# Optimization experiments

Measured on AMD Instinct MI355X. Metric: run time of the kernel, lower is better.

Reference implementation:

```python
import jax, jax.numpy as jnp
import numpy as np

B, T = 256, 512          # sequences, timesteps (batched over pyro.markov loop)
DATA_DIM = 88            # piano-roll tones
HIDDEN_DIM = 16          # HMM latent states
NN_DIM = 48
NN_CHANNELS = 2
KERNEL = 3


def _uniform(key, shape, fan_in):
    bound = 1.0 / np.sqrt(fan_in)
    return jax.random.uniform(key, shape, minval=-bound, maxval=bound, dtype=jnp.float32)


def setup_inputs() -> dict:
    key = jax.random.key(0)
    ks = jax.random.split(key, 13)
    w = jax.random.randint(ks[0], (B, T, 1), 0, HIDDEN_DIM)
    x = jax.random.randint(ks[1], (B, T, 1), 0, HIDDEN_DIM)
    y = jax.random.uniform(ks[2], (B, T, DATA_DIM), dtype=jnp.float32)
    return {
        "w": w, "x": x, "y": y,
        # nn.Linear(hidden_dim, nn_dim) for x and w one-hots
        "W_xh": _uniform(ks[3], (NN_DIM, HIDDEN_DIM), HIDDEN_DIM),
        "b_xh": _uniform(ks[4], (NN_DIM,), HIDDEN_DIM),
        "W_wh": _uniform(ks[5], (NN_DIM, HIDDEN_DIM), HIDDEN_DIM),
        "b_wh": _uniform(ks[6], (NN_DIM,), HIDDEN_DIM),
        # nn.Linear(nn_channels*data_dim, nn_dim)
        "W_yh": _uniform(ks[7], (NN_DIM, NN_CHANNELS * DATA_DIM), NN_CHANNELS * DATA_DIM),
        "b_yh": _uniform(ks[8], (NN_DIM,), NN_CHANNELS * DATA_DIM),
        # nn.Conv1d(1, nn_channels, 3, padding=1)
        "W_conv": _uniform(ks[9], (NN_CHANNELS, 1, KERNEL), KERNEL),
        "b_conv": _uniform(ks[10], (NN_CHANNELS,), KERNEL),
        # nn.Linear(nn_dim, data_dim)
        "W_hl": _uniform(ks[11], (DATA_DIM, NN_DIM), NN_DIM),
        "b_hl": _uniform(ks[12], (DATA_DIM,), NN_DIM),
    }


def _tones_generator(w, x, y, W_xh, b_xh, W_wh, b_wh, W_yh, b_yh, W_conv, b_conv, W_hl, b_hl):
    b, t, d = y.shape
    # one-hot scatter of the latent state indices (trailing index dim of size 1)
    w_onehot = jax.nn.one_hot(w[..., 0], HIDDEN_DIM, dtype=y.dtype)   # [B,T,H]
    x_onehot = jax.nn.one_hot(x[..., 0], HIDDEN_DIM, dtype=y.dtype)   # [B,T,H]
    # Conv1d(1 -> nn_channels, k=3, pad=1) over the tone axis
    y_nch = y.reshape(b * t, 1, d)                                    # [BT,1,D]
    y_conv = jax.lax.conv_general_dilated(
        y_nch, W_conv, window_strides=(1,), padding=[(1, 1)],
        dimension_numbers=("NCH", "OIH", "NCH"))
    y_conv = jax.nn.relu(y_conv + b_conv[None, :, None])              # [BT,C,D]
    y_conv = y_conv.reshape(b, t, NN_CHANNELS * d)                    # [B,T,C*D]
    h = jax.nn.relu(
        jnp.einsum("bth,nh->btn", x_onehot, W_xh) + b_xh
        + jnp.einsum("bth,nh->btn", w_onehot, W_wh) + b_wh
        + jnp.einsum("btc,nc->btn", y_conv, W_yh) + b_yh)             # [B,T,ND]
    return jnp.einsum("btn,dn->btd", h, W_hl) + b_hl                  # [B,T,D]


def reference(w, x, y, W_xh, b_xh, W_wh, b_wh, W_yh, b_yh, W_conv, b_conv, W_hl, b_hl):
    return _tones_generator(w, x, y, W_xh, b_xh, W_wh, b_wh, W_yh, b_yh,
                            W_conv, b_conv, W_hl, b_hl)
```

## Files before the change

### kernel.cpp

```cpp
#include <hip/hip_runtime.h>
#include <stdint.h>

#define NTOK (256 * 512)
#define TPB 256

typedef short bf16x8 __attribute__((ext_vector_type(8)));
typedef float f32x4 __attribute__((ext_vector_type(4)));
typedef unsigned short u16;
typedef unsigned int u32;

#define B1_U16 10752
#define B2_U16 6144

__device__ __forceinline__ u16 f2bf(float f) {
    u32 u = __float_as_uint(f);
    return (u16)((u + 0x7fffu + ((u >> 16) & 1u)) >> 16);
}

__global__ __launch_bounds__(256, 1)
void prep_weights(const float* __restrict__ Wxh, const float* __restrict__ bxh,
                  const float* __restrict__ Wwh, const float* __restrict__ bwh,
                  const float* __restrict__ Wyh, const float* __restrict__ byh,
                  const float* __restrict__ Whl, const float* __restrict__ bhl,
                  u16* __restrict__ ws)
{
    int e = blockIdx.x * 256 + threadIdx.x;
    if (e < B1_U16) {
        int j = e & 7, n = (e >> 3) % 48, kc = e / 384;
        int k = kc * 8 + j;
        float v;
        if (k < 176)       v = Wyh[n * 176 + (k & 1) * 88 + (k >> 1)];
        else if (k < 192)  v = Wxh[n * 16 + (k - 176)];
        else if (k < 208)  v = Wwh[n * 16 + (k - 192)];
        else if (k == 208) v = bxh[n] + bwh[n] + byh[n];
        else               v = 0.0f;
        ws[e] = f2bf(v);
    } else if (e < B1_U16 + B2_U16) {
        int e2 = e - B1_U16;
        int j = e2 & 7, dd = (e2 >> 3) % 96, kc = e2 / 768;
        int k = kc * 8 + j;
        float v = 0.0f;
        if (dd < 88) {
            if (k < 48)       v = Whl[dd * 48 + k];
            else if (k == 48) v = bhl[dd];
        }
        ws[e] = f2bf(v);
    }
}

__global__ __launch_bounds__(256, 2)
void tones_v5(const int* __restrict__ widx, const int* __restrict__ xidx,
              const float* __restrict__ y,
              const float* __restrict__ Wconv, const float* __restrict__ bconv,
              const u16* __restrict__ wsb,
              float* __restrict__ out)
{
    __shared__ __align__(16) u16 sH[4 * 1024];

    const int tid = threadIdx.x;
    const int wave = tid >> 6, lane = tid & 63;
    const int q = lane >> 4, c = lane & 15;

    bf16x8 B1[7][3];
    #pragma unroll
    for (int ks = 0; ks < 7; ks++)
        #pragma unroll
        for (int nt = 0; nt < 3; nt++)
            B1[ks][nt] = *(const bf16x8*)(wsb + ((ks * 4 + q) * 48 + nt * 16 + c) * 8);
    bf16x8 B2[2][6];
    #pragma unroll
    for (int ks = 0; ks < 2; ks++)
        #pragma unroll
        for (int nt = 0; nt < 6; nt++)
            B2[ks][nt] = *(const bf16x8*)(wsb + B1_U16 + ((ks * 4 + q) * 96 + nt * 16 + c) * 8);

    const float wc00 = Wconv[0], wc01 = Wconv[1], wc02 = Wconv[2];
    const float wc10 = Wconv[3], wc11 = Wconv[4], wc12 = Wconv[5];
    const float bc0 = bconv[0], bc1 = bconv[1];

    u16* sW = sH + wave * 1024;

    #pragma unroll 1
    for (int t = 0; t < 4; t++) {
        const int tb = blockIdx.x * 256 + wave * 64 + t * 16;
        const float* yc = y + (size_t)(tb + c) * 88;
        const int xv = xidx[tb + c];
        const int wv = widx[tb + c];

        f32x4 h0 = {0, 0, 0, 0}, h1 = {0, 0, 0, 0}, h2 = {0, 0, 0, 0};

        #pragma unroll
        for (int s = 0; s < 5; s++) {
            const int d0 = 16 * s + 4 * q;
            float p0 = (d0 == 0) ? 0.0f : yc[d0 - 1];
            float4 v4 = *(const float4*)(yc + d0);
            float p5 = yc[d0 + 4];
            float p[6] = {p0, v4.x, v4.y, v4.z, v4.w, p5};
            bf16x8 af;
            #pragma unroll
            for (int i = 0; i < 4; i++) {
                float c0 = fmaf(wc00, p[i], fmaf(wc01, p[i + 1], fmaf(wc02, p[i + 2], bc0)));
                float c1 = fmaf(wc10, p[i], fmaf(wc11, p[i + 1], fmaf(wc12, p[i + 2], bc1)));
                af[2 * i]     = (short)f2bf(fmaxf(c0, 0.0f));
                af[2 * i + 1] = (short)f2bf(fmaxf(c1, 0.0f));
            }
            h0 = __builtin_amdgcn_mfma_f32_16x16x32_bf16(af, B1[s][0], h0, 0, 0, 0);
            h1 = __builtin_amdgcn_mfma_f32_16x16x32_bf16(af, B1[s][1], h1, 0, 0, 0);
            h2 = __builtin_amdgcn_mfma_f32_16x16x32_bf16(af, B1[s][2], h2, 0, 0, 0);
        }
        {
            bf16x8 af;
            if (q < 2) {
                const int d0 = 80 + 4 * q;
                float p0 = yc[d0 - 1];
                float4 v4 = *(const float4*)(yc + d0);
                float p5 = (q == 0) ? yc[84] : 0.0f;
                float p[6] = {p0, v4.x, v4.y, v4.z, v4.w, p5};
                #pragma unroll
                for (int i = 0; i < 4; i++) {
                    float c0 = fmaf(wc00, p[i], fmaf(wc01, p[i + 1], fmaf(wc02, p[i + 2], bc0)));
                    float c1 = fmaf(wc10, p[i], fmaf(wc11, p[i + 1], fmaf(wc12, p[i + 2], bc1)));
                    af[2 * i]     = (short)f2bf(fmaxf(c0, 0.0f));
                    af[2 * i + 1] = (short)f2bf(fmaxf(c1, 0.0f));
                }
            } else {
                const int base = (q - 2) * 8;
                #pragma unroll
                for (int j = 0; j < 8; j++)
                    af[j] = (short)((base + j == xv) ? 0x3F80 : 0);
            }
            h0 = __builtin_amdgcn_mfma_f32_16x16x32_bf16(af, B1[5][0], h0, 0, 0, 0);
            h1 = __builtin_amdgcn_mfma_f32_16x16x32_bf16(af, B1[5][1], h1, 0, 0, 0);
            h2 = __builtin_amdgcn_mfma_f32_16x16x32_bf16(af, B1[5][2], h2, 0, 0, 0);
        }
        {
            bf16x8 af;
            if (q < 2) {
                const int base = q * 8;
                #pragma unroll
                for (int j = 0; j < 8; j++)
                    af[j] = (short)((base + j == wv) ? 0x3F80 : 0);
            } else {
                #pragma unroll
                for (int j = 0; j < 8; j++)
                    af[j] = (short)((q == 2 && j == 0) ? 0x3F80 : 0);
            }
            h0 = __builtin_amdgcn_mfma_f32_16x16x32_bf16(af, B1[6][0], h0, 0, 0, 0);
            h1 = __builtin_amdgcn_mfma_f32_16x16x32_bf16(af, B1[6][1], h1, 0, 0, 0);
            h2 = __builtin_amdgcn_mfma_f32_16x16x32_bf16(af, B1[6][2], h2, 0, 0, 0);
        }

        if (lane < 32) {
            uint4 hz = make_uint4((lane < 16) ? 0x3F80u : 0u, 0, 0, 0);
            *(uint4*)(sW + ((6 + (lane >> 4)) * 16 + (lane & 15)) * 8) = hz;
        }
        #pragma unroll
        for (int r = 0; r < 4; r++) {
            const int row = q * 4 + r;
            sW[((0 + (c >> 3)) * 16 + row) * 8 + (c & 7)] = f2bf(fmaxf(h0[r], 0.0f));
            sW[((2 + (c >> 3)) * 16 + row) * 8 + (c & 7)] = f2bf(fmaxf(h1[r], 0.0f));
            sW[((4 + (c >> 3)) * 16 + row) * 8 + (c & 7)] = f2bf(fmaxf(h2[r], 0.0f));
        }

        f32x4 o0 = {0,0,0,0}, o1 = {0,0,0,0}, o2 = {0,0,0,0};
        f32x4 o3 = {0,0,0,0}, o4 = {0,0,0,0}, o5 = {0,0,0,0};
        #pragma unroll
        for (int ks = 0; ks < 2; ks++) {
            bf16x8 a2 = *(const bf16x8*)(sW + ((ks * 4 + q) * 16 + c) * 8);
            o0 = __builtin_amdgcn_mfma_f32_16x16x32_bf16(a2, B2[ks][0], o0, 0, 0, 0);
            o1 = __builtin_amdgcn_mfma_f32_16x16x32_bf16(a2, B2[ks][1], o1, 0, 0, 0);
            o2 = __builtin_amdgcn_mfma_f32_16x16x32_bf16(a2, B2[ks][2], o2, 0, 0, 0);
            o3 = __builtin_amdgcn_mfma_f32_16x16x32_bf16(a2, B2[ks][3], o3, 0, 0, 0);
            o4 = __builtin_amdgcn_mfma_f32_16x16x32_bf16(a2, B2[ks][4], o4, 0, 0, 0);
            o5 = __builtin_amdgcn_mfma_f32_16x16x32_bf16(a2, B2[ks][5], o5, 0, 0, 0);
        }

        float* orow = out + (size_t)(tb + q * 4) * 88;
        #pragma unroll
        for (int r = 0; r < 4; r++) {
            orow[r * 88 +  0 + c] = o0[r];
            orow[r * 88 + 16 + c] = o1[r];
            orow[r * 88 + 32 + c] = o2[r];
            orow[r * 88 + 48 + c] = o3[r];
            orow[r * 88 + 64 + c] = o4[r];
            if (c < 8) orow[r * 88 + 80 + c] = o5[r];
        }
    }
}

extern "C" void kernel_launch(void* const* d_in, const int* in_sizes, int n_in,
                              void* d_out, int out_size, void* d_ws, size_t ws_size,
                              hipStream_t stream) {
    (void)in_sizes; (void)n_in; (void)out_size; (void)ws_size;
    u16* ws = (u16*)d_ws;
    prep_weights<<<dim3(66), dim3(TPB), 0, stream>>>(
        (const float*)d_in[3],  (const float*)d_in[4],
        (const float*)d_in[5],  (const float*)d_in[6],
        (const float*)d_in[7],  (const float*)d_in[8],
        (const float*)d_in[11], (const float*)d_in[12], ws);
    tones_v5<<<dim3(NTOK / 256), dim3(TPB), 0, stream>>>(
        (const int*)d_in[0], (const int*)d_in[1], (const float*)d_in[2],
        (const float*)d_in[9], (const float*)d_in[10], ws, (float*)d_out);
}
```

Before: 136.5 us.

## Stream weight fragments per k-step and give each wave one 16-token tile

Each wave no longer keeps all B1/B2 weight fragments in registers. It now processes a single 16-token tile and double-buffers the weight fragments from global memory, loading them one k-step ahead. Launch bounds go from 2 to 4 blocks per SM and the grid is four times larger, to raise occupancy and hide latency. Float-to-bf16 conversion switches to the hardware v_cvt_pk_bf16_f32 instruction. The cost is more repeated weight loads (cache hits) per token, and the per-wave loop that amortized the weight loads is removed.

```diff
diff --git a/kernel.cpp b/kernel.cpp
--- a/kernel.cpp
+++ b/kernel.cpp
@@ -15,6 +15,11 @@
 __device__ __forceinline__ u16 f2bf(float f) {
     u32 u = __float_as_uint(f);
     return (u16)((u + 0x7fffu + ((u >> 16) & 1u)) >> 16);
+}
+__device__ __forceinline__ u32 cvtpk(float lo, float hi) {
+    u32 r;
+    asm("v_cvt_pk_bf16_f32 %0, %1, %2" : "=v"(r) : "v"(lo), "v"(hi));
+    return r;
 }
 
 __global__ __launch_bounds__(256, 1)
@@ -48,8 +53,8 @@
     }
 }
 
-__global__ __launch_bounds__(256, 2)
-void tones_v5(const int* __restrict__ widx, const int* __restrict__ xidx,
+__global__ __launch_bounds__(256, 4)
+void tones_v7(const int* __restrict__ widx, const int* __restrict__ xidx,
               const float* __restrict__ y,
               const float* __restrict__ Wconv, const float* __restrict__ bconv,
               const u16* __restrict__ wsb,
@@ -60,56 +65,57 @@
     const int tid = threadIdx.x;
     const int wave = tid >> 6, lane = tid & 63;
     const int q = lane >> 4, c = lane & 15;
-
-    bf16x8 B1[7][3];
-    #pragma unroll
-    for (int ks = 0; ks < 7; ks++)
-        #pragma unroll
-        for (int nt = 0; nt < 3; nt++)
-            B1[ks][nt] = *(const bf16x8*)(wsb + ((ks * 4 + q) * 48 + nt * 16 + c) * 8);
-    bf16x8 B2[2][6];
-    #pragma unroll
-    for (int ks = 0; ks < 2; ks++)
-        #pragma unroll
-        for (int nt = 0; nt < 6; nt++)
-            B2[ks][nt] = *(const bf16x8*)(wsb + B1_U16 + ((ks * 4 + q) * 96 + nt * 16 + c) * 8);
+    u16* sW = sH + wave * 1024;
+
+    const int tb = blockIdx.x * 64 + wave * 16;
+    const float* yc = y + (size_t)(tb + c) * 88;
+    const int xv = xidx[tb + c];
+    const int wv = widx[tb + c];
 
     const float wc00 = Wconv[0], wc01 = Wconv[1], wc02 = Wconv[2];
     const float wc10 = Wconv[3], wc11 = Wconv[4], wc12 = Wconv[5];
     const float bc0 = bconv[0], bc1 = bconv[1];
 
-    u16* sW = sH + wave * 1024;
-
-    #pragma unroll 1
-    for (int t = 0; t < 4; t++) {
-        const int tb = blockIdx.x * 256 + wave * 64 + t * 16;
-        const float* yc = y + (size_t)(tb + c) * 88;
-        const int xv = xidx[tb + c];
-        const int wv = widx[tb + c];
-
-        f32x4 h0 = {0, 0, 0, 0}, h1 = {0, 0, 0, 0}, h2 = {0, 0, 0, 0};
-
-        #pragma unroll
-        for (int s = 0; s < 5; s++) {
-            const int d0 = 16 * s + 4 * q;
+    if (lane < 32) {
+        uint4 hz = make_uint4((lane < 16) ? 0x3F80u : 0u, 0, 0, 0);
+        *(uint4*)(sW + ((6 + (lane >> 4)) * 16 + (lane & 15)) * 8) = hz;
+    }
+
+    f32x4 h0 = {0, 0, 0, 0}, h1 = {0, 0, 0, 0}, h2 = {0, 0, 0, 0};
+
+    const u16* bp1 = wsb + (q * 48 + c) * 8;
+    const u16* bp2 = wsb + B1_U16 + (q * 96 + c) * 8;
+
+    bf16x8 gA[3], gB[3];
+    gA[0] = *(const bf16x8*)(bp1 + 0 * 8);
+    gA[1] = *(const bf16x8*)(bp1 + 16 * 8);
+    gA[2] = *(const bf16x8*)(bp1 + 32 * 8);
+
+    #pragma unroll
+    for (int ks = 0; ks < 7; ks++) {
+        bf16x8* cur = (ks & 1) ? gB : gA;
+        bf16x8* nxt = (ks & 1) ? gA : gB;
+        if (ks < 6) {
+            nxt[0] = *(const bf16x8*)(bp1 + ((ks + 1) * 192 +  0) * 8);
+            nxt[1] = *(const bf16x8*)(bp1 + ((ks + 1) * 192 + 16) * 8);
+            nxt[2] = *(const bf16x8*)(bp1 + ((ks + 1) * 192 + 32) * 8);
+        }
+        bf16x8 af;
+        if (ks < 5) {
+            const int d0 = 16 * ks + 4 * q;
             float p0 = (d0 == 0) ? 0.0f : yc[d0 - 1];
             float4 v4 = *(const float4*)(yc + d0);
             float p5 = yc[d0 + 4];
             float p[6] = {p0, v4.x, v4.y, v4.z, v4.w, p5};
-            bf16x8 af;
             #pragma unroll
             for (int i = 0; i < 4; i++) {
                 float c0 = fmaf(wc00, p[i], fmaf(wc01, p[i + 1], fmaf(wc02, p[i + 2], bc0)));
                 float c1 = fmaf(wc10, p[i], fmaf(wc11, p[i + 1], fmaf(wc12, p[i + 2], bc1)));
-                af[2 * i]     = (short)f2bf(fmaxf(c0, 0.0f));
-                af[2 * i + 1] = (short)f2bf(fmaxf(c1, 0.0f));
+                u32 pk = cvtpk(fmaxf(c0, 0.0f), fmaxf(c1, 0.0f));
+                af[2 * i]     = (short)(pk & 0xFFFF);
+                af[2 * i + 1] = (short)(pk >> 16);
             }
-            h0 = __builtin_amdgcn_mfma_f32_16x16x32_bf16(af, B1[s][0], h0, 0, 0, 0);
-            h1 = __builtin_amdgcn_mfma_f32_16x16x32_bf16(af, B1[s][1], h1, 0, 0, 0);
-            h2 = __builtin_amdgcn_mfma_f32_16x16x32_bf16(af, B1[s][2], h2, 0, 0, 0);
-        }
-        {
-            bf16x8 af;
+        } else if (ks == 5) {
             if (q < 2) {
                 const int d0 = 80 + 4 * q;
                 float p0 = yc[d0 - 1];
@@ -120,8 +126,9 @@
                 for (int i = 0; i < 4; i++) {
                     float c0 = fmaf(wc00, p[i], fmaf(wc01, p[i + 1], fmaf(wc02, p[i + 2], bc0)));
                     float c1 = fmaf(wc10, p[i], fmaf(wc11, p[i + 1], fmaf(wc12, p[i + 2], bc1)));
-                    af[2 * i]     = (short)f2bf(fmaxf(c0, 0.0f));
-                    af[2 * i + 1] = (short)f2bf(fmaxf(c1, 0.0f));
+                    u32 pk = cvtpk(fmaxf(c0, 0.0f), fmaxf(c1, 0.0f));
+                    af[2 * i]     = (short)(pk & 0xFFFF);
+                    af[2 * i + 1] = (short)(pk >> 16);
                 }
             } else {
                 const int base = (q - 2) * 8;
@@ -129,12 +136,7 @@
                 for (int j = 0; j < 8; j++)
                     af[j] = (short)((base + j == xv) ? 0x3F80 : 0);
             }
-            h0 = __builtin_amdgcn_mfma_f32_16x16x32_bf16(af, B1[5][0], h0, 0, 0, 0);
-            h1 = __builtin_amdgcn_mfma_f32_16x16x32_bf16(af, B1[5][1], h1, 0, 0, 0);
-            h2 = __builtin_amdgcn_mfma_f32_16x16x32_bf16(af, B1[5][2], h2, 0, 0, 0);
-        }
-        {
-            bf16x8 af;
+        } else {
             if (q < 2) {
                 const int base = q * 8;
                 #pragma unroll
@@ -145,46 +147,59 @@
                 for (int j = 0; j < 8; j++)
                     af[j] = (short)((q == 2 && j == 0) ? 0x3F80 : 0);
             }
-            h0 = __builtin_amdgcn_mfma_f32_16x16x32_bf16(af, B1[6][0], h0, 0, 0, 0);
-            h1 = __builtin_amdgcn_mfma_f32_16x16x32_bf16(af, B1[6][1], h1, 0, 0, 0);
-            h2 = __builtin_amdgcn_mfma_f32_16x16x32_bf16(af, B1[6][2], h2, 0, 0, 0);
         }
-
-        if (lane < 32) {
-            uint4 hz = make_uint4((lane < 16) ? 0x3F80u : 0u, 0, 0, 0);
-            *(uint4*)(sW + ((6 + (lane >> 4)) * 16 + (lane & 15)) * 8) = hz;
-        }
-        #pragma unroll
-        for (int r = 0; r < 4; r++) {
-            const int row = q * 4 + r;
-            sW[((0 + (c >> 3)) * 16 + row) * 8 + (c & 7)] = f2bf(fmaxf(h0[r], 0.0f));
-            sW[((2 + (c >> 3)) * 16 + row) * 8 + (c & 7)] = f2bf(fmaxf(h1[r], 0.0f));
-            sW[((4 + (c >> 3)) * 16 + row) * 8 + (c & 7)] = f2bf(fmaxf(h2[r], 0.0f));
-        }
-
-        f32x4 o0 = {0,0,0,0}, o1 = {0,0,0,0}, o2 = {0,0,0,0};
-        f32x4 o3 = {0,0,0,0}, o4 = {0,0,0,0}, o5 = {0,0,0,0};
-        #pragma unroll
-        for (int ks = 0; ks < 2; ks++) {
-            bf16x8 a2 = *(const bf16x8*)(sW + ((ks * 4 + q) * 16 + c) * 8);
-            o0 = __builtin_amdgcn_mfma_f32_16x16x32_bf16(a2, B2[ks][0], o0, 0, 0, 0);
-            o1 = __builtin_amdgcn_mfma_f32_16x16x32_bf16(a2, B2[ks][1], o1, 0, 0, 0);
-            o2 = __builtin_amdgcn_mfma_f32_16x16x32_bf16(a2, B2[ks][2], o2, 0, 0, 0);
-            o3 = __builtin_amdgcn_mfma_f32_16x16x32_bf16(a2, B2[ks][3], o3, 0, 0, 0);
-            o4 = __builtin_amdgcn_mfma_f32_16x16x32_bf16(a2, B2[ks][4], o4, 0, 0, 0);
-            o5 = __builtin_amdgcn_mfma_f32_16x16x32_bf16(a2, B2[ks][5], o5, 0, 0, 0);
-        }
-
-        float* orow = out + (size_t)(tb + q * 4) * 88;
-        #pragma unroll
-        for (int r = 0; r < 4; r++) {
-            orow[r * 88 +  0 + c] = o0[r];
-            orow[r * 88 + 16 + c] = o1[r];
-            orow[r * 88 + 32 + c] = o2[r];
-            orow[r * 88 + 48 + c] = o3[r];
-            orow[r * 88 + 64 + c] = o4[r];
-            if (c < 8) orow[r * 88 + 80 + c] = o5[r];
-        }
+        h0 = __builtin_amdgcn_mfma_f32_16x16x32_bf16(af, cur[0], h0, 0, 0, 0);
+        h1 = __builtin_amdgcn_mfma_f32_16x16x32_bf16(af, cur[1], h1, 0, 0, 0);
+        h2 = __builtin_amdgcn_mfma_f32_16x16x32_bf16(af, cur[2], h2, 0, 0, 0);
+    }
+
+    bf16x8 b2a[6], b2b[6];
+    #pragma unroll
+    for (int nt = 0; nt < 6; nt++)
+        b2a[nt] = *(const bf16x8*)(bp2 + (nt * 16) * 8);
+
+    #pragma unroll
+    for (int r = 0; r < 4; r++) {
+        const int row = q * 4 + r;
+        sW[((0 + (c >> 3)) * 16 + row) * 8 + (c & 7)] = (u16)cvtpk(fmaxf(h0[r], 0.0f), 0.0f);
+        sW[((2 + (c >> 3)) * 16 + row) * 8 + (c & 7)] = (u16)cvtpk(fmaxf(h1[r], 0.0f), 0.0f);
+        sW[((4 + (c >> 3)) * 16 + row) * 8 + (c & 7)] = (u16)cvtpk(fmaxf(h2[r], 0.0f), 0.0f);
+    }
+
+    #pragma unroll
+    for (int nt = 0; nt < 6; nt++)
+        b2b[nt] = *(const bf16x8*)(bp2 + (384 + nt * 16) * 8);
+
+    f32x4 o0 = {0,0,0,0}, o1 = {0,0,0,0}, o2 = {0,0,0,0};
+    f32x4 o3 = {0,0,0,0}, o4 = {0,0,0,0}, o5 = {0,0,0,0};
+    {
+        bf16x8 a2 = *(const bf16x8*)(sW + (q * 16 + c) * 8);
+        o0 = __builtin_amdgcn_mfma_f32_16x16x32_bf16(a2, b2a[0], o0, 0, 0, 0);
+        o1 = __builtin_amdgcn_mfma_f32_16x16x32_bf16(a2, b2a[1], o1, 0, 0, 0);
+        o2 = __builtin_amdgcn_mfma_f32_16x16x32_bf16(a2, b2a[2], o2, 0, 0, 0);
+        o3 = __builtin_amdgcn_mfma_f32_16x16x32_bf16(a2, b2a[3], o3, 0, 0, 0);
+        o4 = __builtin_amdgcn_mfma_f32_16x16x32_bf16(a2, b2a[4], o4, 0, 0, 0);
+        o5 = __builtin_amdgcn_mfma_f32_16x16x32_bf16(a2, b2a[5], o5, 0, 0, 0);
+    }
+    {
+        bf16x8 a2 = *(const bf16x8*)(sW + ((4 + q) * 16 + c) * 8);
+        o0 = __builtin_amdgcn_mfma_f32_16x16x32_bf16(a2, b2b[0], o0, 0, 0, 0);
+        o1 = __builtin_amdgcn_mfma_f32_16x16x32_bf16(a2, b2b[1], o1, 0, 0, 0);
+        o2 = __builtin_amdgcn_mfma_f32_16x16x32_bf16(a2, b2b[2], o2, 0, 0, 0);
+        o3 = __builtin_amdgcn_mfma_f32_16x16x32_bf16(a2, b2b[3], o3, 0, 0, 0);
+        o4 = __builtin_amdgcn_mfma_f32_16x16x32_bf16(a2, b2b[4], o4, 0, 0, 0);
+        o5 = __builtin_amdgcn_mfma_f32_16x16x32_bf16(a2, b2b[5], o5, 0, 0, 0);
+    }
+
+    float* orow = out + (size_t)(tb + q * 4) * 88;
+    #pragma unroll
+    for (int r = 0; r < 4; r++) {
+        orow[r * 88 +  0 + c] = o0[r];
+        orow[r * 88 + 16 + c] = o1[r];
+        orow[r * 88 + 32 + c] = o2[r];
+        orow[r * 88 + 48 + c] = o3[r];
+        orow[r * 88 + 64 + c] = o4[r];
+        if (c < 8) orow[r * 88 + 80 + c] = o5[r];
     }
 }
 
@@ -198,7 +213,7 @@
         (const float*)d_in[5],  (const float*)d_in[6],
         (const float*)d_in[7],  (const float*)d_in[8],
         (const float*)d_in[11], (const float*)d_in[12], ws);
-    tones_v5<<<dim3(NTOK / 256), dim3(TPB), 0, stream>>>(
+    tones_v7<<<dim3(NTOK / 64), dim3(TPB), 0, stream>>>(
         (const int*)d_in[0], (const int*)d_in[1], (const float*)d_in[2],
         (const float*)d_in[9], (const float*)d_in[10], ws, (float*)d_out);
 }
```

Measured after the change: 136.5 us. About the same (-0.1%).
